# Performance work log

Hardware: AMD Instinct MI355X
Metric: run time of the kernel (lower is better)

## Reference

```python
import jax, jax.numpy as jnp
import numpy as np
import math

H_SP, W_SP = 200, 200          # BEV spatial shape (single level, m == h)
D_MODEL = 256
N_HEADS = 8
N_POINTS = 4
D_HEAD = D_MODEL // N_HEADS


def _grid_init_bias():
    # Matches TemporalSelfAttention._reset_parameters for sampling_offsets.bias
    thetas = np.arange(N_HEADS, dtype=np.float32) * (2.0 * np.pi / N_HEADS)
    grid = np.stack([np.cos(thetas), np.sin(thetas)], -1)
    grid = grid / np.abs(grid).max(-1, keepdims=True)
    grid = np.tile(grid[:, None, None, :], (1, 1, N_POINTS, 1))  # (NH, 1, P, 2)
    for i in range(N_POINTS):
        grid[:, :, i, :] *= (i + 1)
    return jnp.asarray(grid.reshape(-1), dtype=jnp.float32)


def setup_inputs() -> dict:
    key = jax.random.key(0)
    ks = jax.random.split(key, 10)
    N = 1
    Lq = H_SP * W_SP
    Lin = H_SP * W_SP
    xav = math.sqrt(6.0 / (2 * D_MODEL))
    query = jax.random.normal(ks[0], (N, Lq, D_MODEL), jnp.float32)
    query_pos = jax.random.normal(ks[1], (N, Lq, D_MODEL), jnp.float32)
    reference_points = jax.random.uniform(ks[2], (N, Lq, 1, 2), jnp.float32)
    input_flatten = jax.random.normal(ks[3], (N, Lin, D_MODEL), jnp.float32)
    W_value = jax.random.uniform(ks[4], (D_MODEL, D_MODEL), jnp.float32, -xav, xav)
    b_value = jnp.zeros((D_MODEL,), jnp.float32)
    # small random weights (trained-model-like) + canonical grid bias
    W_off = jax.random.normal(ks[5], (N_HEADS * N_POINTS * 2, D_MODEL), jnp.float32) * 0.005
    b_off = _grid_init_bias()
    W_attn = jax.random.normal(ks[6], (N_HEADS * N_POINTS, D_MODEL), jnp.float32) * 0.02
    b_attn = jnp.zeros((N_HEADS * N_POINTS,), jnp.float32)
    W_out = jax.random.uniform(ks[7], (D_MODEL, D_MODEL), jnp.float32, -xav, xav)
    b_out = jnp.zeros((D_MODEL,), jnp.float32)
    return dict(query=query, query_pos=query_pos, reference_points=reference_points,
                input_flatten=input_flatten, W_value=W_value, b_value=b_value,
                W_off=W_off, b_off=b_off, W_attn=W_attn, b_attn=b_attn,
                W_out=W_out, b_out=b_out)


def _bilinear_sample(vflat, x, y):
    # vflat: (N, NH, H*W, DH); x, y: (N, NH, K) pixel coords (align_corners=False)
    # Zero padding outside the feature map, matching the MSDeformAttn CUDA kernel.
    x0f = jnp.floor(x)
    y0f = jnp.floor(y)
    x0 = x0f.astype(jnp.int32)
    y0 = y0f.astype(jnp.int32)
    lw = x - x0f
    lh = y - y0f
    gather = jax.vmap(jax.vmap(lambda v, i: v[i]))  # over batch, head
    acc = jnp.zeros(x.shape + (vflat.shape[-1],), vflat.dtype)
    corners = ((y0, x0, (1.0 - lh) * (1.0 - lw)),
               (y0, x0 + 1, (1.0 - lh) * lw),
               (y0 + 1, x0, lh * (1.0 - lw)),
               (y0 + 1, x0 + 1, lh * lw))
    for yi, xi, wgt in corners:
        valid = ((xi >= 0) & (xi < W_SP) & (yi >= 0) & (yi < H_SP)).astype(vflat.dtype)
        idx = jnp.clip(yi, 0, H_SP - 1) * W_SP + jnp.clip(xi, 0, W_SP - 1)
        g = gather(vflat, idx)                      # (N, NH, K, DH)
        acc = acc + (wgt * valid)[..., None] * g
    return acc


def reference(query, query_pos, reference_points, input_flatten,
              W_value, b_value, W_off, b_off, W_attn, b_attn, W_out, b_out):
    N, Lq, _ = query.shape
    q = query + query_pos
    value = input_flatten @ W_value.T + b_value                     # (N, Lin, D)
    value = value.reshape(N, -1, N_HEADS, D_HEAD).transpose(0, 2, 1, 3)  # (N, NH, Lin, DH)
    off = (q @ W_off.T + b_off).reshape(N, Lq, N_HEADS, N_POINTS, 2)
    attn = jax.nn.softmax((q @ W_attn.T + b_attn).reshape(N, Lq, N_HEADS, N_POINTS), axis=-1)
    norm = jnp.array([W_SP, H_SP], jnp.float32)                      # offset_normalizer (w, h)
    ref = reference_points[:, :, 0, :][:, :, None, None, :]          # (N, Lq, 1, 1, 2)
    loc = ref + off / norm                                           # (N, Lq, NH, P, 2) in [0,1]
    x = (loc[..., 0] * W_SP - 0.5).transpose(0, 2, 1, 3).reshape(N, N_HEADS, Lq * N_POINTS)
    y = (loc[..., 1] * H_SP - 0.5).transpose(0, 2, 1, 3).reshape(N, N_HEADS, Lq * N_POINTS)
    sampled = _bilinear_sample(value, x, y).reshape(N, N_HEADS, Lq, N_POINTS, D_HEAD)
    out = jnp.einsum('nhqpd,nqhp->nqhd', sampled, attn).reshape(N, Lq, D_MODEL)
    return out @ W_out.T + b_out
```

## Files before the change

kernel.cpp:

```cpp
#include <hip/hip_runtime.h>
#include <math.h>

#define LQ 40000
#define DMODEL 256
#define NHD 8
#define NPT 4
#define DHD 32
#define HSP 200
#define WSP 200

typedef short s16x8 __attribute__((ext_vector_type(8)));
typedef float f32x4 __attribute__((ext_vector_type(4)));

__device__ __forceinline__ unsigned short f2b(float f) {
    unsigned u = __builtin_bit_cast(unsigned, f);
    u += 0x7FFFu + ((u >> 16) & 1u);
    return (unsigned short)(u >> 16);
}
__device__ __forceinline__ float b2f(unsigned short u) {
    return __builtin_bit_cast(float, ((unsigned)u) << 16);
}
__device__ __forceinline__ void pk8(const float4& v0, const float4& v1,
                                    unsigned short* o) {
    o[0] = f2b(v0.x); o[1] = f2b(v0.y); o[2] = f2b(v0.z); o[3] = f2b(v0.w);
    o[4] = f2b(v1.x); o[5] = f2b(v1.y); o[6] = f2b(v1.z); o[7] = f2b(v1.w);
}


__global__ __launch_bounds__(256) void convert_weights(
    const float* __restrict__ Wv, const float* __restrict__ Woff,
    const float* __restrict__ Wattn, const float* __restrict__ Wout,
    unsigned short* __restrict__ dst)
{
    int u = blockIdx.x * 256 + threadIdx.x;
    int lane = u & 63, ks = (u >> 6) & 7, slot = u >> 9;
    int l15 = lane & 15, quad = lane >> 4;
    const float* src;
    if (slot < 16) {
        src = Wv + (size_t)(slot * 16 + l15) * 256;
    } else if (slot < 22) {
        int col = (slot - 16) * 16 + l15;
        src = (col < 64) ? Woff + (size_t)col * 256
                         : Wattn + (size_t)(col - 64) * 256;
    } else {
        src = Wout + (size_t)((slot - 22) * 16 + l15) * 256;
    }
    int k0 = ks * 32 + quad * 8;
    float4 v0 = *(const float4*)(src + k0);
    float4 v1 = *(const float4*)(src + k0 + 4);
    union { unsigned short u16[8]; uint4 v; } tmp;
    pk8(v0, v1, tmp.u16);
    *(uint4*)(dst + (size_t)u * 8) = tmp.v;
}

template <bool HasA2>
__global__ __launch_bounds__(256) void transpose_a(
    const float* __restrict__ A, const float* __restrict__ A2,
    unsigned short* __restrict__ dst)
{
    const int strip = blockIdx.x;
    const int w = threadIdx.x >> 6, lane = threadIdx.x & 63;
    const int l15 = lane & 15, quad = lane >> 4;
    const size_t rowoff = ((size_t)strip * 16 + l15) * 256;
#pragma unroll
    for (int i = 0; i < 2; ++i) {
        int ks = w * 2 + i;
        int k0 = ks * 32 + quad * 8;
        float4 v0 = *(const float4*)(A + rowoff + k0);
        float4 v1 = *(const float4*)(A + rowoff + k0 + 4);
        if constexpr (HasA2) {
            float4 w0 = *(const float4*)(A2 + rowoff + k0);
            float4 w1 = *(const float4*)(A2 + rowoff + k0 + 4);
            v0.x += w0.x; v0.y += w0.y; v0.z += w0.z; v0.w += w0.w;
            v1.x += w1.x; v1.y += w1.y; v1.z += w1.z; v1.w += w1.w;
        }
        union { unsigned short u16[8]; uint4 v; } tmp;
        pk8(v0, v1, tmp.u16);
        *(uint4*)(dst + (size_t)strip * 4096 + ks * 512 + lane * 8) = tmp.v;
    }
}

template <int NT, int TPW, int CMODE>
__global__ __launch_bounds__(256, 2) void gemm_rs(
    const unsigned short* __restrict__ Af, const unsigned short* __restrict__ Wf,
    const float* __restrict__ b1, const float* __restrict__ b2, int split,
    void* __restrict__ Cv)
{
    const int t = threadIdx.x;
    const int wave = t >> 6, lane = t & 63;
    const int l15 = lane & 15, quad = lane >> 4;

    s16x8 bf[TPW][8];
    float bias[TPW];
#pragma unroll
    for (int j = 0; j < TPW; ++j) {
        bias[j] = 0.f;
        int c = wave * TPW + j;
        if (c < NT) {
#pragma unroll
            for (int ks = 0; ks < 8; ++ks)
                bf[j][ks] = *(const s16x8*)&Wf[(size_t)(c * 8 + ks) * 512 + lane * 8];
            int col = c * 16 + l15;
            bias[j] = (col < split) ? b1[col] : b2[col - split];
        }
    }

#pragma unroll
    for (int s = 0; s < 2; ++s) {
        const size_t g = (size_t)blockIdx.x * 2 + s;
        s16x8 a[8];
#pragma unroll
        for (int ks = 0; ks < 8; ++ks)
            a[ks] = *(const s16x8*)&Af[g * 4096 + ks * 512 + lane * 8];
#pragma unroll
        for (int j = 0; j < TPW; ++j) {
            int c = wave * TPW + j;
            if (c < NT) {
                f32x4 acc = (f32x4){0.f, 0.f, 0.f, 0.f};
#pragma unroll
                for (int ks = 0; ks < 8; ++ks)
                    acc = __builtin_amdgcn_mfma_f32_16x16x32_bf16(a[ks], bf[j][ks],
                                                                  acc, 0, 0, 0);
#pragma unroll
                for (int r2 = 0; r2 < 4; ++r2) {
                    size_t row = g * 16 + quad * 4 + r2;
                    float v = acc[r2] + bias[j];
                    if constexpr (CMODE == 1) {
                        ((unsigned short*)Cv)[(((size_t)(c >> 1) * LQ + row) << 5)
                                              + ((c & 1) << 4) + l15] = f2b(v);
                    } else {
                        ((float*)Cv)[row * (NT * 16) + c * 16 + l15] = v;
                    }
                }
            }
        }
    }
}

__global__ __launch_bounds__(256) void sample_kernel(
    const float* __restrict__ raw, const float* __restrict__ rp,
    const unsigned short* __restrict__ value, unsigned short* __restrict__ outa)
{
    __shared__ int4   sIdx[8][8][4];
    __shared__ float4 sW[8][8][4];

    const int t = threadIdx.x;
    {
        const int qi = t >> 5, h = (t >> 2) & 7, p = t & 3;
        const int q = blockIdx.x * 8 + qi;
        const float* r = raw + (size_t)q * 96;
        float l0 = r[64 + h * 4 + 0], l1 = r[64 + h * 4 + 1];
        float l2 = r[64 + h * 4 + 2], l3 = r[64 + h * 4 + 3];
        float mx = fmaxf(fmaxf(l0, l1), fmaxf(l2, l3));
        float e0 = __expf(l0 - mx), e1 = __expf(l1 - mx);
        float e2 = __expf(l2 - mx), e3 = __expf(l3 - mx);
        float inv = 1.f / (e0 + e1 + e2 + e3);
        float ep = (p == 0) ? e0 : (p == 1) ? e1 : (p == 2) ? e2 : e3;
        float wp = ep * inv;

        float x = rp[(size_t)q * 2 + 0] * (float)WSP - 0.5f + r[h * 8 + p * 2 + 0];
        float y = rp[(size_t)q * 2 + 1] * (float)HSP - 0.5f + r[h * 8 + p * 2 + 1];
        float x0f = floorf(x), y0f = floorf(y);
        int x0 = (int)x0f, y0 = (int)y0f;
        float lw = x - x0f, lh = y - y0f;
        float cw[4] = {(1.f - lh) * (1.f - lw), (1.f - lh) * lw,
                       lh * (1.f - lw), lh * lw};
        int4 I; float4 W;
        int* Ip = &I.x; float* Wp = &W.x;
#pragma unroll
        for (int c = 0; c < 4; ++c) {
            int cx = x0 + (c & 1), cy = y0 + (c >> 1);
            bool valid = (cx >= 0) & (cx < WSP) & (cy >= 0) & (cy < HSP);
            int ccx = cx < 0 ? 0 : (cx > WSP - 1 ? WSP - 1 : cx);
            int ccy = cy < 0 ? 0 : (cy > HSP - 1 ? HSP - 1 : cy);
            Ip[c] = (ccy * WSP + ccx) * DHD;
            Wp[c] = valid ? cw[c] * wp : 0.f;
        }
        sIdx[qi][h][p] = I;
        sW[qi][h][p] = W;
    }
    __syncthreads();

    const int qq = t >> 6, h = (t >> 3) & 7, d8 = t & 7;
    const unsigned short* vp = value + (size_t)h * LQ * DHD + d8 * 4;
#pragma unroll
    for (int e = 0; e < 2; ++e) {
        int qi = qq * 2 + e;
        float a0 = 0.f, a1 = 0.f, a2 = 0.f, a3 = 0.f;
#pragma unroll
        for (int p = 0; p < 4; ++p) {
            int4 I = sIdx[qi][h][p];
            float4 W = sW[qi][h][p];
            uint2 g0 = *(const uint2*)(vp + I.x);
            uint2 g1 = *(const uint2*)(vp + I.y);
            uint2 g2 = *(const uint2*)(vp + I.z);
            uint2 g3 = *(const uint2*)(vp + I.w);
            a0 += W.x * b2f((unsigned short)g0.x);
            a1 += W.x * b2f((unsigned short)(g0.x >> 16));
            a2 += W.x * b2f((unsigned short)g0.y);
            a3 += W.x * b2f((unsigned short)(g0.y >> 16));
            a0 += W.y * b2f((unsigned short)g1.x);
            a1 += W.y * b2f((unsigned short)(g1.x >> 16));
            a2 += W.y * b2f((unsigned short)g1.y);
            a3 += W.y * b2f((unsigned short)(g1.y >> 16));
            a0 += W.z * b2f((unsigned short)g2.x);
            a1 += W.z * b2f((unsigned short)(g2.x >> 16));
            a2 += W.z * b2f((unsigned short)g2.y);
            a3 += W.z * b2f((unsigned short)(g2.y >> 16));
            a0 += W.w * b2f((unsigned short)g3.x);
            a1 += W.w * b2f((unsigned short)(g3.x >> 16));
            a2 += W.w * b2f((unsigned short)g3.y);
            a3 += W.w * b2f((unsigned short)(g3.y >> 16));
        }
        int q = blockIdx.x * 8 + qi;
        size_t off = (size_t)(q >> 4) * 4096 + h * 512 + (d8 >> 1) * 128
                   + (q & 15) * 8 + (d8 & 1) * 4;
        union { unsigned short u16[4]; uint2 v; } o;
        o.u16[0] = f2b(a0); o.u16[1] = f2b(a1);
        o.u16[2] = f2b(a2); o.u16[3] = f2b(a3);
        *(uint2*)&outa[off] = o.v;
    }
}

extern "C" void kernel_launch(void* const* d_in, const int* in_sizes, int n_in,
                              void* d_out, int out_size, void* d_ws, size_t ws_size,
                              hipStream_t stream)
{
    const float* query         = (const float*)d_in[0];
    const float* query_pos     = (const float*)d_in[1];
    const float* ref_points    = (const float*)d_in[2];
    const float* input_flatten = (const float*)d_in[3];
    const float* W_value       = (const float*)d_in[4];
    const float* b_value       = (const float*)d_in[5];
    const float* W_off         = (const float*)d_in[6];
    const float* b_off         = (const float*)d_in[7];
    const float* W_attn        = (const float*)d_in[8];
    const float* b_attn        = (const float*)d_in[9];
    const float* W_out         = (const float*)d_in[10];
    const float* b_out         = (const float*)d_in[11];
    float* out = (float*)d_out;

    unsigned short* val  = (unsigned short*)d_ws;
    float*          raw  = (float*)(val + (size_t)LQ * DMODEL);
    unsigned short* outa = (unsigned short*)(raw + (size_t)LQ * 96);
    unsigned short* Abuf = outa + (size_t)LQ * DMODEL;
    unsigned short* wf   = Abuf + (size_t)LQ * DMODEL;
    unsigned short* wfv  = wf;
    unsigned short* wfoa = wf + 65536;
    unsigned short* wfo  = wf + 90112;

    dim3 blk(256);

    convert_weights<<<dim3(76), blk, 0, stream>>>(W_value, W_off, W_attn, W_out, wf);

    transpose_a<false><<<dim3(LQ / 16), blk, 0, stream>>>(input_flatten, nullptr, Abuf);
    gemm_rs<16, 4, 1><<<dim3(LQ / 32), blk, 0, stream>>>(
        Abuf, wfv, b_value, b_value, 256, val);

    transpose_a<true><<<dim3(LQ / 16), blk, 0, stream>>>(query, query_pos, Abuf);
    gemm_rs<6, 2, 0><<<dim3(LQ / 32), blk, 0, stream>>>(
        Abuf, wfoa, b_off, b_attn, 64, raw);

    sample_kernel<<<dim3(LQ / 8), blk, 0, stream>>>(raw, ref_points, val, outa);

    gemm_rs<16, 4, 0><<<dim3(LQ / 32), blk, 0, stream>>>(
        outa, wfo, b_out, b_out, 256, out);
}
```

Before: 259.2 us.

## Fuse fp32-to-bf16 conversion into GEMMs and make sampling head-major

Removes the separate transpose/convert kernels by loading fp32 activations (and adding query_pos) directly inside the GEMM, packing them to bf16 in registers. This drops a full intermediate bf16 buffer write and read for each of the two input GEMMs. The offset/attention GEMM now writes a head-major 12-float record per query, and the sampling kernel is restructured so each block handles one head over 64 queries, which improves locality of value gathers within a head's slab. The trade-off is that every wave in the fused GEMMs reloads the fp32 A rows redundantly, and the scattered output writes for the new layout are less coalesced.

```diff
diff --git a/kernel.cpp b/kernel.cpp
--- a/kernel.cpp
+++ b/kernel.cpp
@@ -53,36 +53,10 @@
     *(uint4*)(dst + (size_t)u * 8) = tmp.v;
 }
 
-template <bool HasA2>
-__global__ __launch_bounds__(256) void transpose_a(
+template <int NT, int TPW, int CMODE, bool HasA2>
+__global__ __launch_bounds__(256, 2) void gemm_fused(
     const float* __restrict__ A, const float* __restrict__ A2,
-    unsigned short* __restrict__ dst)
-{
-    const int strip = blockIdx.x;
-    const int w = threadIdx.x >> 6, lane = threadIdx.x & 63;
-    const int l15 = lane & 15, quad = lane >> 4;
-    const size_t rowoff = ((size_t)strip * 16 + l15) * 256;
-#pragma unroll
-    for (int i = 0; i < 2; ++i) {
-        int ks = w * 2 + i;
-        int k0 = ks * 32 + quad * 8;
-        float4 v0 = *(const float4*)(A + rowoff + k0);
-        float4 v1 = *(const float4*)(A + rowoff + k0 + 4);
-        if constexpr (HasA2) {
-            float4 w0 = *(const float4*)(A2 + rowoff + k0);
-            float4 w1 = *(const float4*)(A2 + rowoff + k0 + 4);
-            v0.x += w0.x; v0.y += w0.y; v0.z += w0.z; v0.w += w0.w;
-            v1.x += w1.x; v1.y += w1.y; v1.z += w1.z; v1.w += w1.w;
-        }
-        union { unsigned short u16[8]; uint4 v; } tmp;
-        pk8(v0, v1, tmp.u16);
-        *(uint4*)(dst + (size_t)strip * 4096 + ks * 512 + lane * 8) = tmp.v;
-    }
-}
-
-template <int NT, int TPW, int CMODE>
-__global__ __launch_bounds__(256, 2) void gemm_rs(
-    const unsigned short* __restrict__ Af, const unsigned short* __restrict__ Wf,
+    const unsigned short* __restrict__ Wf,
     const float* __restrict__ b1, const float* __restrict__ b2, int split,
     void* __restrict__ Cv)
 {
@@ -108,10 +82,23 @@
 #pragma unroll
     for (int s = 0; s < 2; ++s) {
         const size_t g = (size_t)blockIdx.x * 2 + s;
+        const size_t rowoff = (g * 16 + l15) * 256;
         s16x8 a[8];
 #pragma unroll
-        for (int ks = 0; ks < 8; ++ks)
-            a[ks] = *(const s16x8*)&Af[g * 4096 + ks * 512 + lane * 8];
+        for (int ks = 0; ks < 8; ++ks) {
+            int k0 = ks * 32 + quad * 8;
+            float4 v0 = *(const float4*)(A + rowoff + k0);
+            float4 v1 = *(const float4*)(A + rowoff + k0 + 4);
+            if constexpr (HasA2) {
+                float4 w0 = *(const float4*)(A2 + rowoff + k0);
+                float4 w1 = *(const float4*)(A2 + rowoff + k0 + 4);
+                v0.x += w0.x; v0.y += w0.y; v0.z += w0.z; v0.w += w0.w;
+                v1.x += w1.x; v1.y += w1.y; v1.z += w1.z; v1.w += w1.w;
+            }
+            union { unsigned short u16[8]; s16x8 v; } tmp;
+            pk8(v0, v1, tmp.u16);
+            a[ks] = tmp.v;
+        }
 #pragma unroll
         for (int j = 0; j < TPW; ++j) {
             int c = wave * TPW + j;
@@ -128,6 +115,12 @@
                     if constexpr (CMODE == 1) {
                         ((unsigned short*)Cv)[(((size_t)(c >> 1) * LQ + row) << 5)
                                               + ((c & 1) << 4) + l15] = f2b(v);
+                    } else if constexpr (CMODE == 2) {
+                        int col = c * 16 + l15;
+                        int hh, jj;
+                        if (col < 64) { hh = col >> 3; jj = col & 7; }
+                        else          { hh = (col - 64) >> 2; jj = 8 + (col & 3); }
+                        ((float*)Cv)[((size_t)hh * LQ + row) * 12 + jj] = v;
                     } else {
                         ((float*)Cv)[row * (NT * 16) + c * 16 + l15] = v;
                     }
@@ -137,20 +130,65 @@
     }
 }
 
+template <int NT, int TPW>
+__global__ __launch_bounds__(256, 2) void gemm_rs(
+    const unsigned short* __restrict__ Af, const unsigned short* __restrict__ Wf,
+    const float* __restrict__ b1, float* __restrict__ C)
+{
+    const int t = threadIdx.x;
+    const int wave = t >> 6, lane = t & 63;
+    const int l15 = lane & 15, quad = lane >> 4;
+
+    s16x8 bf[TPW][8];
+    float bias[TPW];
+#pragma unroll
+    for (int j = 0; j < TPW; ++j) {
+        int c = wave * TPW + j;
+#pragma unroll
+        for (int ks = 0; ks < 8; ++ks)
+            bf[j][ks] = *(const s16x8*)&Wf[(size_t)(c * 8 + ks) * 512 + lane * 8];
+        bias[j] = b1[c * 16 + l15];
+    }
+
+#pragma unroll
+    for (int s = 0; s < 2; ++s) {
+        const size_t g = (size_t)blockIdx.x * 2 + s;
+        s16x8 a[8];
+#pragma unroll
+        for (int ks = 0; ks < 8; ++ks)
+            a[ks] = *(const s16x8*)&Af[g * 4096 + ks * 512 + lane * 8];
+#pragma unroll
+        for (int j = 0; j < TPW; ++j) {
+            int c = wave * TPW + j;
+            f32x4 acc = (f32x4){0.f, 0.f, 0.f, 0.f};
+#pragma unroll
+            for (int ks = 0; ks < 8; ++ks)
+                acc = __builtin_amdgcn_mfma_f32_16x16x32_bf16(a[ks], bf[j][ks],
+                                                              acc, 0, 0, 0);
+#pragma unroll
+            for (int r2 = 0; r2 < 4; ++r2) {
+                size_t row = g * 16 + quad * 4 + r2;
+                C[row * (NT * 16) + c * 16 + l15] = acc[r2] + bias[j];
+            }
+        }
+    }
+}
+
 __global__ __launch_bounds__(256) void sample_kernel(
-    const float* __restrict__ raw, const float* __restrict__ rp,
+    const float* __restrict__ raw2, const float* __restrict__ rp,
     const unsigned short* __restrict__ value, unsigned short* __restrict__ outa)
 {
-    __shared__ int4   sIdx[8][8][4];
-    __shared__ float4 sW[8][8][4];
-
+    __shared__ int4   sIdx[64][4];
+    __shared__ float4 sW[64][4];
+
+    const int h = blockIdx.x & 7;
+    const int q0 = (blockIdx.x >> 3) * 64;
     const int t = threadIdx.x;
     {
-        const int qi = t >> 5, h = (t >> 2) & 7, p = t & 3;
-        const int q = blockIdx.x * 8 + qi;
-        const float* r = raw + (size_t)q * 96;
-        float l0 = r[64 + h * 4 + 0], l1 = r[64 + h * 4 + 1];
-        float l2 = r[64 + h * 4 + 2], l3 = r[64 + h * 4 + 3];
+        const int qi = t >> 2, p = t & 3;
+        const int q = q0 + qi;
+        const float* r = raw2 + ((size_t)h * LQ + q) * 12;
+        float l0 = r[8], l1 = r[9], l2 = r[10], l3 = r[11];
         float mx = fmaxf(fmaxf(l0, l1), fmaxf(l2, l3));
         float e0 = __expf(l0 - mx), e1 = __expf(l1 - mx);
         float e2 = __expf(l2 - mx), e3 = __expf(l3 - mx);
@@ -158,8 +196,8 @@
         float ep = (p == 0) ? e0 : (p == 1) ? e1 : (p == 2) ? e2 : e3;
         float wp = ep * inv;
 
-        float x = rp[(size_t)q * 2 + 0] * (float)WSP - 0.5f + r[h * 8 + p * 2 + 0];
-        float y = rp[(size_t)q * 2 + 1] * (float)HSP - 0.5f + r[h * 8 + p * 2 + 1];
+        float x = rp[(size_t)q * 2 + 0] * (float)WSP - 0.5f + r[p * 2 + 0];
+        float y = rp[(size_t)q * 2 + 1] * (float)HSP - 0.5f + r[p * 2 + 1];
         float x0f = floorf(x), y0f = floorf(y);
         int x0 = (int)x0f, y0 = (int)y0f;
         float lw = x - x0f, lh = y - y0f;
@@ -176,21 +214,21 @@
             Ip[c] = (ccy * WSP + ccx) * DHD;
             Wp[c] = valid ? cw[c] * wp : 0.f;
         }
-        sIdx[qi][h][p] = I;
-        sW[qi][h][p] = W;
+        sIdx[qi][p] = I;
+        sW[qi][p] = W;
     }
     __syncthreads();
 
-    const int qq = t >> 6, h = (t >> 3) & 7, d8 = t & 7;
+    const int d8 = t & 7, qp = t >> 3;
     const unsigned short* vp = value + (size_t)h * LQ * DHD + d8 * 4;
 #pragma unroll
     for (int e = 0; e < 2; ++e) {
-        int qi = qq * 2 + e;
+        int qi = qp * 2 + e;
         float a0 = 0.f, a1 = 0.f, a2 = 0.f, a3 = 0.f;
 #pragma unroll
         for (int p = 0; p < 4; ++p) {
-            int4 I = sIdx[qi][h][p];
-            float4 W = sW[qi][h][p];
+            int4 I = sIdx[qi][p];
+            float4 W = sW[qi][p];
             uint2 g0 = *(const uint2*)(vp + I.x);
             uint2 g1 = *(const uint2*)(vp + I.y);
             uint2 g2 = *(const uint2*)(vp + I.z);
@@ -212,7 +250,7 @@
             a2 += W.w * b2f((unsigned short)g3.y);
             a3 += W.w * b2f((unsigned short)(g3.y >> 16));
         }
-        int q = blockIdx.x * 8 + qi;
+        int q = q0 + qi;
         size_t off = (size_t)(q >> 4) * 4096 + h * 512 + (d8 >> 1) * 128
                    + (q & 15) * 8 + (d8 & 1) * 4;
         union { unsigned short u16[4]; uint2 v; } o;
@@ -241,10 +279,9 @@
     float* out = (float*)d_out;
 
     unsigned short* val  = (unsigned short*)d_ws;
-    float*          raw  = (float*)(val + (size_t)LQ * DMODEL);
-    unsigned short* outa = (unsigned short*)(raw + (size_t)LQ * 96);
-    unsigned short* Abuf = outa + (size_t)LQ * DMODEL;
-    unsigned short* wf   = Abuf + (size_t)LQ * DMODEL;
+    float*          raw2 = (float*)(val + (size_t)LQ * DMODEL);
+    unsigned short* outa = (unsigned short*)(raw2 + (size_t)LQ * 96);
+    unsigned short* wf   = outa + (size_t)LQ * DMODEL;
     unsigned short* wfv  = wf;
     unsigned short* wfoa = wf + 65536;
     unsigned short* wfo  = wf + 90112;
@@ -253,16 +290,13 @@
 
     convert_weights<<<dim3(76), blk, 0, stream>>>(W_value, W_off, W_attn, W_out, wf);
 
-    transpose_a<false><<<dim3(LQ / 16), blk, 0, stream>>>(input_flatten, nullptr, Abuf);
-    gemm_rs<16, 4, 1><<<dim3(LQ / 32), blk, 0, stream>>>(
-        Abuf, wfv, b_value, b_value, 256, val);
-
-    transpose_a<true><<<dim3(LQ / 16), blk, 0, stream>>>(query, query_pos, Abuf);
-    gemm_rs<6, 2, 0><<<dim3(LQ / 32), blk, 0, stream>>>(
-        Abuf, wfoa, b_off, b_attn, 64, raw);
-
-    sample_kernel<<<dim3(LQ / 8), blk, 0, stream>>>(raw, ref_points, val, outa);
-
-    gemm_rs<16, 4, 0><<<dim3(LQ / 32), blk, 0, stream>>>(
-        outa, wfo, b_out, b_out, 256, out);
-}
+    gemm_fused<16, 4, 1, false><<<dim3(LQ / 32), blk, 0, stream>>>(
+        input_flatten, nullptr, wfv, b_value, b_value, 256, val);
+
+    gemm_fused<6, 2, 2, true><<<dim3(LQ / 32), blk, 0, stream>>>(
+        query, query_pos, wfoa, b_off, b_attn, 64, raw2);
+
+    sample_kernel<<<dim3(8 * (LQ / 64)), blk, 0, stream>>>(raw2, ref_points, val, outa);
+
+    gemm_rs<16, 4><<<dim3(LQ / 32), blk, 0, stream>>>(outa, wfo, b_out, out);
+}
```

New measurement: 259.7 us. Within noise of the previous version (+0.2%).
